# Optimization experiments

Measured on AMD Instinct MI355X. Metric: run time of the kernel, lower is better.

The kernel has to match this reference:

```python
import jax, jax.numpy as jnp
import numpy as np

# JAX reference for BERN-NN-Implicit LayerModule.forward.
# Semantics: for each output node i,
#   combined_over[i]  = sum_j relu(W)[i,j]*inputs_over[j] + (-relu(-W))[i,j]*inputs_under[j] + bias[i]
#   combined_under[i] = sum_j (-relu(-W))[i,j]*inputs_over[j] + relu(W)[i,j]*inputs_under[j] + bias[i]
# With all input Bernstein polynomials at equal degree, SumModule reduces to addition
# and prod_input_weights reduces to a weighted sum over the previous-layer neuron axis.

N_IN = 64      # previous-layer neurons
SIZE = 64      # nodes in this layer
G = 513        # Bernstein coefficient grid per dim (degree 512 + 1), dims = 2


def setup_inputs() -> dict:
    key = jax.random.key(0)
    k1, k2, k3, k4 = jax.random.split(key, 4)
    return {
        "inputs_under": jax.random.normal(k1, (N_IN, G, G), dtype=jnp.float32),
        "inputs_over": jax.random.normal(k2, (N_IN, G, G), dtype=jnp.float32),
        "weights": jax.random.normal(k3, (SIZE, N_IN), dtype=jnp.float32),
        "biases": jax.random.normal(k4, (SIZE,), dtype=jnp.float32),
        "layer_idx": 0,
    }


def reference(inputs_under, inputs_over, weights, biases, layer_idx):
    w_pos = jax.nn.relu(weights)          # [size, n_in]
    w_neg = -jax.nn.relu(-weights)        # [size, n_in]
    b = biases[:, None, None]             # [size, 1, 1]
    # [size, G, G] Bernstein coefficient grids per output node
    combined_over = (jnp.einsum("oi,ixy->oxy", w_pos, inputs_over)
                     + jnp.einsum("oi,ixy->oxy", w_neg, inputs_under)) + b
    combined_under = (jnp.einsum("oi,ixy->oxy", w_neg, inputs_over)
                      + jnp.einsum("oi,ixy->oxy", w_pos, inputs_under)) + b
    return combined_under, combined_over
```

## Files before the change

kernel.cpp:

```cpp
#include <hip/hip_runtime.h>

constexpr int PIX   = 513 * 513;
constexpr int NTILE = 128;
constexpr int NFULL = PIX / NTILE;
constexpr int GRID  = 512;

typedef short bf16x8 __attribute__((ext_vector_type(8)));
typedef float f32x4  __attribute__((ext_vector_type(4)));

__device__ __forceinline__ unsigned short f2bf(float f) {
    unsigned u = __builtin_bit_cast(unsigned, f);
    u += 0x7fffu + ((u >> 16) & 1u);
    return (unsigned short)(u >> 16);
}
__device__ __forceinline__ unsigned pack2(float a, float b) {
    return (unsigned)f2bf(a) | ((unsigned)f2bf(b) << 16);
}

__global__ __launch_bounds__(512, 2) void mfma_bounds_kernel(
    const float* __restrict__ under,
    const float* __restrict__ over,
    const float* __restrict__ W,
    const float* __restrict__ bias,
    float* __restrict__ out_under,
    float* __restrict__ out_over)
{
    __shared__ alignas(16) unsigned short Xt[2][NTILE * 128];

    const int t    = threadIdx.x;
    const int wv   = t >> 6;
    const int lane = t & 63;
    const int lrow = lane & 15;
    const int lg   = lane >> 4;
    const int m0   = wv * 16;

    bf16x8 A[4];
    {
        const int m = m0 + lrow;
        const float* wr = W + (m & 63) * 64;
        #pragma unroll
        for (int ks = 0; ks < 4; ++ks) {
            const int kbase = ks * 32 + lg * 8;
            const bool same = ((kbase < 64) == (m < 64));
            const float4 wa = *(const float4*)(wr + (kbase & 63));
            const float4 wb = *(const float4*)(wr + (kbase & 63) + 4);
            bf16x8 f;
            f[0] = (short)f2bf(same ? fmaxf(wa.x, 0.f) : fminf(wa.x, 0.f));
            f[1] = (short)f2bf(same ? fmaxf(wa.y, 0.f) : fminf(wa.y, 0.f));
            f[2] = (short)f2bf(same ? fmaxf(wa.z, 0.f) : fminf(wa.z, 0.f));
            f[3] = (short)f2bf(same ? fmaxf(wa.w, 0.f) : fminf(wa.w, 0.f));
            f[4] = (short)f2bf(same ? fmaxf(wb.x, 0.f) : fminf(wb.x, 0.f));
            f[5] = (short)f2bf(same ? fmaxf(wb.y, 0.f) : fminf(wb.y, 0.f));
            f[6] = (short)f2bf(same ? fmaxf(wb.z, 0.f) : fminf(wb.z, 0.f));
            f[7] = (short)f2bf(same ? fmaxf(wb.w, 0.f) : fminf(wb.w, 0.f));
            A[ks] = f;
        }
    }
    float bb[4];
    #pragma unroll
    for (int r = 0; r < 4; ++r)
        bb[r] = bias[(m0 + lg * 4 + r) & 63];

    const int q   = t & 31;
    const int ro  = t >> 5;
    const float* src = (ro < 8) ? over : under;
    const int rr  = (ro & 7) * 8;
    const int px0 = q * 4;
    const int kb  = ro * 16;
    const int xwr = lrow << 4;

    int tile = blockIdx.x;
    f32x4 ld[8];
    {
        const size_t pb = (size_t)tile * NTILE + px0;
        #pragma unroll
        for (int j = 0; j < 8; ++j)
            ld[j] = *(const f32x4*)(src + (size_t)(rr + j) * PIX + pb);
    }

    int cur = 0;
    while (tile < NFULL) {
        #pragma unroll
        for (int c = 0; c < 4; ++c) {
            int4 pk;
            pk.x = (int)pack2(ld[0][c], ld[1][c]);
            pk.y = (int)pack2(ld[2][c], ld[3][c]);
            pk.z = (int)pack2(ld[4][c], ld[5][c]);
            pk.w = (int)pack2(ld[6][c], ld[7][c]);
            const int px  = px0 + c;
            const int off = px * 256 + (kb ^ ((px & 15) << 4));
            *(int4*)((char*)&Xt[cur][0] + off) = pk;
        }

        const int pxbase    = tile * NTILE;
        const int tile_next = tile + GRID;

        if (tile_next < NFULL) {
            const size_t pb = (size_t)tile_next * NTILE + px0;
            #pragma unroll
            for (int j = 0; j < 8; ++j)
                ld[j] = *(const f32x4*)(src + (size_t)(rr + j) * PIX + pb);
        }

        __syncthreads();

        f32x4 acc[8];
        #pragma unroll
        for (int nt = 0; nt < 8; ++nt) {
            f32x4 v = {bb[0], bb[1], bb[2], bb[3]};
            acc[nt] = v;
        }
        #pragma unroll
        for (int nt = 0; nt < 8; ++nt) {
            const int prow = nt * 16 + lrow;
            bf16x8 Bf[4];
            #pragma unroll
            for (int ks = 0; ks < 4; ++ks) {
                const int ch = ks * 4 + lg;
                Bf[ks] = *(const bf16x8*)((const char*)&Xt[cur][0] +
                           prow * 256 + ((ch * 16) ^ xwr));
            }
            #pragma unroll
            for (int ks = 0; ks < 4; ++ks)
                acc[nt] = __builtin_amdgcn_mfma_f32_16x16x32_bf16(
                    A[ks], Bf[ks], acc[nt], 0, 0, 0);
        }

        #pragma unroll
        for (int r = 0; r < 4; ++r) {
            const int m = m0 + lg * 4 + r;
            float* base = (m < 64) ? (out_over  + (size_t)m        * PIX)
                                   : (out_under + (size_t)(m - 64) * PIX);
            #pragma unroll
            for (int nt = 0; nt < 8; ++nt)
                __builtin_nontemporal_store(acc[nt][r],
                    base + pxbase + nt * 16 + lrow);
        }

        cur ^= 1;
        tile = tile_next;
    }

    if (blockIdx.x == GRID - 1 && t < 128) {
        const int p = NFULL * NTILE;
        const int m = t;
        const int o = m & 63;
        const float* prim = (m < 64) ? over  : under;
        const float* sec  = (m < 64) ? under : over;
        float acc = bias[o];
        for (int i = 0; i < 64; ++i) {
            const float w = W[o * 64 + i];
            acc += fmaxf(w, 0.f) * prim[(size_t)i * PIX + p]
                 + fminf(w, 0.f) * sec [(size_t)i * PIX + p];
        }
        if (m < 64) out_over [(size_t)m        * PIX + p] = acc;
        else        out_under[(size_t)(m - 64) * PIX + p] = acc;
    }
}

extern "C" void kernel_launch(void* const* d_in, const int* in_sizes, int n_in,
                              void* d_out, int out_size, void* d_ws, size_t ws_size,
                              hipStream_t stream) {
    const float* under = (const float*)d_in[0];
    const float* over  = (const float*)d_in[1];
    const float* W     = (const float*)d_in[2];
    const float* bias  = (const float*)d_in[3];
    float* out_under = (float*)d_out;
    float* out_over  = out_under + (size_t)64 * PIX;

    mfma_bounds_kernel<<<GRID, 512, 0, stream>>>(under, over, W, bias,
                                                 out_under, out_over);
}
```

Before: 88.41 us.

## Warp-specialize loader and MFMA waves with fixed tiles per block

Splits each block into four producer waves that load fp32 inputs, convert them to bf16 and write them into double-buffered LDS, and four consumer waves that each compute two 16-row M tiles with MFMA and store the outputs. The grid becomes NFULL/4 blocks, each handling four consecutive tiles instead of grid-striding over 512 persistent blocks. The goal is to overlap global loads with the compute and store phases through specialization. The trade-off is that half the waves do no MFMA work, producers hold 16 registers of loads each, and there are more blocks with a short prologue each.

```diff
diff --git a/kernel.cpp b/kernel.cpp
--- a/kernel.cpp
+++ b/kernel.cpp
@@ -3,7 +3,8 @@
 constexpr int PIX   = 513 * 513;
 constexpr int NTILE = 128;
 constexpr int NFULL = PIX / NTILE;
-constexpr int GRID  = 512;
+constexpr int TPB   = 4;
+constexpr int GRID  = NFULL / TPB;
 
 typedef short bf16x8 __attribute__((ext_vector_type(8)));
 typedef float f32x4  __attribute__((ext_vector_type(4)));
@@ -27,118 +28,130 @@
 {
     __shared__ alignas(16) unsigned short Xt[2][NTILE * 128];
 
-    const int t    = threadIdx.x;
-    const int wv   = t >> 6;
-    const int lane = t & 63;
-    const int lrow = lane & 15;
-    const int lg   = lane >> 4;
-    const int m0   = wv * 16;
+    const int t   = threadIdx.x;
+    const int wv  = t >> 6;
+    const int tb0 = blockIdx.x * TPB;
 
-    bf16x8 A[4];
-    {
-        const int m = m0 + lrow;
-        const float* wr = W + (m & 63) * 64;
-        #pragma unroll
-        for (int ks = 0; ks < 4; ++ks) {
-            const int kbase = ks * 32 + lg * 8;
-            const bool same = ((kbase < 64) == (m < 64));
-            const float4 wa = *(const float4*)(wr + (kbase & 63));
-            const float4 wb = *(const float4*)(wr + (kbase & 63) + 4);
-            bf16x8 f;
-            f[0] = (short)f2bf(same ? fmaxf(wa.x, 0.f) : fminf(wa.x, 0.f));
-            f[1] = (short)f2bf(same ? fmaxf(wa.y, 0.f) : fminf(wa.y, 0.f));
-            f[2] = (short)f2bf(same ? fmaxf(wa.z, 0.f) : fminf(wa.z, 0.f));
-            f[3] = (short)f2bf(same ? fmaxf(wa.w, 0.f) : fminf(wa.w, 0.f));
-            f[4] = (short)f2bf(same ? fmaxf(wb.x, 0.f) : fminf(wb.x, 0.f));
-            f[5] = (short)f2bf(same ? fmaxf(wb.y, 0.f) : fminf(wb.y, 0.f));
-            f[6] = (short)f2bf(same ? fmaxf(wb.z, 0.f) : fminf(wb.z, 0.f));
-            f[7] = (short)f2bf(same ? fmaxf(wb.w, 0.f) : fminf(wb.w, 0.f));
-            A[ks] = f;
-        }
-    }
-    float bb[4];
-    #pragma unroll
-    for (int r = 0; r < 4; ++r)
-        bb[r] = bias[(m0 + lg * 4 + r) & 63];
+    if (wv < 4) {
+        const int q   = t & 31;
+        const int ro  = t >> 5;
+        const float* src = (ro < 4) ? over : under;
+        const int rr  = (ro & 3) * 16;
+        const int px0 = q * 4;
 
-    const int q   = t & 31;
-    const int ro  = t >> 5;
-    const float* src = (ro < 8) ? over : under;
-    const int rr  = (ro & 7) * 8;
-    const int px0 = q * 4;
-    const int kb  = ro * 16;
-    const int xwr = lrow << 4;
-
-    int tile = blockIdx.x;
-    f32x4 ld[8];
-    {
-        const size_t pb = (size_t)tile * NTILE + px0;
-        #pragma unroll
-        for (int j = 0; j < 8; ++j)
-            ld[j] = *(const f32x4*)(src + (size_t)(rr + j) * PIX + pb);
-    }
-
-    int cur = 0;
-    while (tile < NFULL) {
-        #pragma unroll
-        for (int c = 0; c < 4; ++c) {
-            int4 pk;
-            pk.x = (int)pack2(ld[0][c], ld[1][c]);
-            pk.y = (int)pack2(ld[2][c], ld[3][c]);
-            pk.z = (int)pack2(ld[4][c], ld[5][c]);
-            pk.w = (int)pack2(ld[6][c], ld[7][c]);
-            const int px  = px0 + c;
-            const int off = px * 256 + (kb ^ ((px & 15) << 4));
-            *(int4*)((char*)&Xt[cur][0] + off) = pk;
+#define STAGE(i)                                                               \
+        {                                                                      \
+            const size_t pb = (size_t)(tb0 + (i)) * NTILE + px0;               \
+            f32x4 ld[16];                                                      \
+            _Pragma("unroll")                                                  \
+            for (int j = 0; j < 16; ++j)                                       \
+                ld[j] = *(const f32x4*)(src + (size_t)(rr + j) * PIX + pb);    \
+            char* bw = (char*)&Xt[(i) & 1][0];                                 \
+            _Pragma("unroll")                                                  \
+            for (int c = 0; c < 4; ++c) {                                      \
+                const int px = px0 + c;                                        \
+                const int xw = (px & 15) << 4;                                 \
+                _Pragma("unroll")                                              \
+                for (int oct = 0; oct < 2; ++oct) {                            \
+                    int4 pk;                                                   \
+                    pk.x = (int)pack2(ld[oct*8+0][c], ld[oct*8+1][c]);         \
+                    pk.y = (int)pack2(ld[oct*8+2][c], ld[oct*8+3][c]);         \
+                    pk.z = (int)pack2(ld[oct*8+4][c], ld[oct*8+5][c]);         \
+                    pk.w = (int)pack2(ld[oct*8+6][c], ld[oct*8+7][c]);         \
+                    const int kbyte = ro * 32 + oct * 16;                      \
+                    *(int4*)(bw + px * 256 + (kbyte ^ xw)) = pk;               \
+                }                                                              \
+            }                                                                  \
         }
 
-        const int pxbase    = tile * NTILE;
-        const int tile_next = tile + GRID;
+        STAGE(0);
+        __syncthreads();
+        #pragma unroll 1
+        for (int i = 0; i < TPB; ++i) {
+            if (i + 1 < TPB) STAGE(i + 1);
+            __syncthreads();
+        }
+#undef STAGE
+    } else {
+        const int lane = t & 63;
+        const int lrow = lane & 15;
+        const int lg   = lane >> 4;
+        const int m0   = (wv - 4) * 32;
 
-        if (tile_next < NFULL) {
-            const size_t pb = (size_t)tile_next * NTILE + px0;
+        bf16x8 A[2][4];
+        #pragma unroll
+        for (int mt = 0; mt < 2; ++mt) {
+            const int m = m0 + mt * 16 + lrow;
+            const float* wr = W + (m & 63) * 64;
             #pragma unroll
-            for (int j = 0; j < 8; ++j)
-                ld[j] = *(const f32x4*)(src + (size_t)(rr + j) * PIX + pb);
+            for (int ks = 0; ks < 4; ++ks) {
+                const int kbase = ks * 32 + lg * 8;
+                const bool same = ((kbase < 64) == (m < 64));
+                const float4 wa = *(const float4*)(wr + (kbase & 63));
+                const float4 wb = *(const float4*)(wr + (kbase & 63) + 4);
+                bf16x8 f;
+                f[0] = (short)f2bf(same ? fmaxf(wa.x, 0.f) : fminf(wa.x, 0.f));
+                f[1] = (short)f2bf(same ? fmaxf(wa.y, 0.f) : fminf(wa.y, 0.f));
+                f[2] = (short)f2bf(same ? fmaxf(wa.z, 0.f) : fminf(wa.z, 0.f));
+                f[3] = (short)f2bf(same ? fmaxf(wa.w, 0.f) : fminf(wa.w, 0.f));
+                f[4] = (short)f2bf(same ? fmaxf(wb.x, 0.f) : fminf(wb.x, 0.f));
+                f[5] = (short)f2bf(same ? fmaxf(wb.y, 0.f) : fminf(wb.y, 0.f));
+                f[6] = (short)f2bf(same ? fmaxf(wb.z, 0.f) : fminf(wb.z, 0.f));
+                f[7] = (short)f2bf(same ? fmaxf(wb.w, 0.f) : fminf(wb.w, 0.f));
+                A[mt][ks] = f;
+            }
         }
+        float bb[2][4];
+        #pragma unroll
+        for (int mt = 0; mt < 2; ++mt)
+            #pragma unroll
+            for (int r = 0; r < 4; ++r)
+                bb[mt][r] = bias[(m0 + mt * 16 + lg * 4 + r) & 63];
 
         __syncthreads();
 
-        f32x4 acc[8];
-        #pragma unroll
-        for (int nt = 0; nt < 8; ++nt) {
-            f32x4 v = {bb[0], bb[1], bb[2], bb[3]};
-            acc[nt] = v;
+        const int xwr = lrow << 4;
+
+        #pragma unroll 1
+        for (int i = 0; i < TPB; ++i) {
+            const char* br   = (const char*)&Xt[i & 1][0];
+            const int pxbase = (tb0 + i) * NTILE;
+
+            #pragma unroll
+            for (int mt = 0; mt < 2; ++mt) {
+                f32x4 acc[8];
+                #pragma unroll
+                for (int nt = 0; nt < 8; ++nt) {
+                    f32x4 v = {bb[mt][0], bb[mt][1], bb[mt][2], bb[mt][3]};
+                    acc[nt] = v;
+                }
+                #pragma unroll
+                for (int nt = 0; nt < 8; ++nt) {
+                    const int prow = nt * 16 + lrow;
+                    bf16x8 Bf[4];
+                    #pragma unroll
+                    for (int ks = 0; ks < 4; ++ks) {
+                        const int ch = ks * 4 + lg;
+                        Bf[ks] = *(const bf16x8*)(br + prow * 256 + ((ch * 16) ^ xwr));
+                    }
+                    #pragma unroll
+                    for (int ks = 0; ks < 4; ++ks)
+                        acc[nt] = __builtin_amdgcn_mfma_f32_16x16x32_bf16(
+                            A[mt][ks], Bf[ks], acc[nt], 0, 0, 0);
+                }
+                #pragma unroll
+                for (int r = 0; r < 4; ++r) {
+                    const int m = m0 + mt * 16 + lg * 4 + r;
+                    float* base = (m < 64) ? (out_over  + (size_t)m        * PIX)
+                                           : (out_under + (size_t)(m - 64) * PIX);
+                    #pragma unroll
+                    for (int nt = 0; nt < 8; ++nt)
+                        __builtin_nontemporal_store(acc[nt][r],
+                            base + pxbase + nt * 16 + lrow);
+                }
+            }
+            __syncthreads();
         }
-        #pragma unroll
-        for (int nt = 0; nt < 8; ++nt) {
-            const int prow = nt * 16 + lrow;
-            bf16x8 Bf[4];
-            #pragma unroll
-            for (int ks = 0; ks < 4; ++ks) {
-                const int ch = ks * 4 + lg;
-                Bf[ks] = *(const bf16x8*)((const char*)&Xt[cur][0] +
-                           prow * 256 + ((ch * 16) ^ xwr));
-            }
-            #pragma unroll
-            for (int ks = 0; ks < 4; ++ks)
-                acc[nt] = __builtin_amdgcn_mfma_f32_16x16x32_bf16(
-                    A[ks], Bf[ks], acc[nt], 0, 0, 0);
-        }
-
-        #pragma unroll
-        for (int r = 0; r < 4; ++r) {
-            const int m = m0 + lg * 4 + r;
-            float* base = (m < 64) ? (out_over  + (size_t)m        * PIX)
-                                   : (out_under + (size_t)(m - 64) * PIX);
-            #pragma unroll
-            for (int nt = 0; nt < 8; ++nt)
-                __builtin_nontemporal_store(acc[nt][r],
-                    base + pxbase + nt * 16 + lrow);
-        }
-
-        cur ^= 1;
-        tile = tile_next;
     }
 
     if (blockIdx.x == GRID - 1 && t < 128) {
```

Result: slower. 109.5 us (+23.9%).

## Halve block size, compute two M-tiles per wave, interleave LDS packing with MFMA

Applied to the files above, without the earlier changes.

The block shrinks from 512 to 256 threads. Each wave now covers two 16-row output tiles with two sets of weight fragments, and each thread loads 16 input rows instead of 8. The main loop is restructured so that packing the next tile into the other LDS buffer is interleaved between the two MFMA compute phases. This leaves one barrier per iteration, placed after both compute and pack, aiming to overlap LDS writes and global-load latency with matrix math. In exchange, register use per thread rises (16 prefetch vectors and two accumulator sets), and each CU may hold fewer resident waves, which could reduce memory-level parallelism in this bandwidth-bound kernel.

```diff
diff --git a/kernel.cpp b/kernel.cpp
--- a/kernel.cpp
+++ b/kernel.cpp
@@ -17,7 +17,7 @@
     return (unsigned)f2bf(a) | ((unsigned)f2bf(b) << 16);
 }
 
-__global__ __launch_bounds__(512, 2) void mfma_bounds_kernel(
+__global__ __launch_bounds__(256, 2) void mfma_bounds_kernel(
     const float* __restrict__ under,
     const float* __restrict__ over,
     const float* __restrict__ W,
@@ -32,11 +32,12 @@
     const int lane = t & 63;
     const int lrow = lane & 15;
     const int lg   = lane >> 4;
-    const int m0   = wv * 16;
+    const int m0   = wv * 32;
 
-    bf16x8 A[4];
-    {
-        const int m = m0 + lrow;
+    bf16x8 A[2][4];
+    #pragma unroll
+    for (int mt = 0; mt < 2; ++mt) {
+        const int m = m0 + mt * 16 + lrow;
         const float* wr = W + (m & 63) * 64;
         #pragma unroll
         for (int ks = 0; ks < 4; ++ks) {
@@ -53,93 +54,114 @@
             f[5] = (short)f2bf(same ? fmaxf(wb.y, 0.f) : fminf(wb.y, 0.f));
             f[6] = (short)f2bf(same ? fmaxf(wb.z, 0.f) : fminf(wb.z, 0.f));
             f[7] = (short)f2bf(same ? fmaxf(wb.w, 0.f) : fminf(wb.w, 0.f));
-            A[ks] = f;
+            A[mt][ks] = f;
         }
     }
-    float bb[4];
+    float bb[2][4];
     #pragma unroll
-    for (int r = 0; r < 4; ++r)
-        bb[r] = bias[(m0 + lg * 4 + r) & 63];
+    for (int mt = 0; mt < 2; ++mt)
+        #pragma unroll
+        for (int r = 0; r < 4; ++r)
+            bb[mt][r] = bias[(m0 + mt * 16 + lg * 4 + r) & 63];
 
     const int q   = t & 31;
     const int ro  = t >> 5;
-    const float* src = (ro < 8) ? over : under;
-    const int rr  = (ro & 7) * 8;
+    const float* src = (ro < 4) ? over : under;
+    const int rr  = (ro & 3) * 16;
     const int px0 = q * 4;
-    const int kb  = ro * 16;
     const int xwr = lrow << 4;
 
+#define PACK_OCT(b, oct)                                                     \
+    {                                                                        \
+        char* bw = (char*)&Xt[(b)][0];                                       \
+        _Pragma("unroll")                                                    \
+        for (int c = 0; c < 4; ++c) {                                        \
+            const int px = px0 + c;                                          \
+            const int xw = (px & 15) << 4;                                   \
+            int4 pk;                                                         \
+            pk.x = (int)pack2(ld[(oct)*8 + 0][c], ld[(oct)*8 + 1][c]);       \
+            pk.y = (int)pack2(ld[(oct)*8 + 2][c], ld[(oct)*8 + 3][c]);       \
+            pk.z = (int)pack2(ld[(oct)*8 + 4][c], ld[(oct)*8 + 5][c]);       \
+            pk.w = (int)pack2(ld[(oct)*8 + 6][c], ld[(oct)*8 + 7][c]);       \
+            const int kbyte = ro * 32 + (oct) * 16;                          \
+            *(int4*)(bw + px * 256 + (kbyte ^ xw)) = pk;                     \
+        }                                                                    \
+    }
+
+#define COMPUTE_MT(mt)                                                       \
+    {                                                                        \
+        f32x4 acc[8];                                                        \
+        _Pragma("unroll")                                                    \
+        for (int nt = 0; nt < 8; ++nt) {                                     \
+            f32x4 v = {bb[mt][0], bb[mt][1], bb[mt][2], bb[mt][3]};          \
+            acc[nt] = v;                                                     \
+        }                                                                    \
+        _Pragma("unroll")                                                    \
+        for (int nt = 0; nt < 8; ++nt) {                                     \
+            const int prow = nt * 16 + lrow;                                 \
+            bf16x8 Bf[4];                                                    \
+            _Pragma("unroll")                                                \
+            for (int ks = 0; ks < 4; ++ks) {                                 \
+                const int ch = ks * 4 + lg;                                  \
+                Bf[ks] = *(const bf16x8*)(br + prow * 256 + ((ch * 16) ^ xwr)); \
+            }                                                                \
+            _Pragma("unroll")                                                \
+            for (int ks = 0; ks < 4; ++ks)                                   \
+                acc[nt] = __builtin_amdgcn_mfma_f32_16x16x32_bf16(           \
+                    A[mt][ks], Bf[ks], acc[nt], 0, 0, 0);                    \
+        }                                                                    \
+        _Pragma("unroll")                                                    \
+        for (int r = 0; r < 4; ++r) {                                        \
+            const int m = m0 + (mt) * 16 + lg * 4 + r;                       \
+            float* base = (m < 64) ? (out_over  + (size_t)m        * PIX)    \
+                                   : (out_under + (size_t)(m - 64) * PIX);   \
+            _Pragma("unroll")                                                \
+            for (int nt = 0; nt < 8; ++nt)                                   \
+                __builtin_nontemporal_store(acc[nt][r],                      \
+                    base + pxbase + nt * 16 + lrow);                         \
+        }                                                                    \
+    }
+
     int tile = blockIdx.x;
-    f32x4 ld[8];
     {
+        f32x4 ld[16];
         const size_t pb = (size_t)tile * NTILE + px0;
         #pragma unroll
-        for (int j = 0; j < 8; ++j)
+        for (int j = 0; j < 16; ++j)
             ld[j] = *(const f32x4*)(src + (size_t)(rr + j) * PIX + pb);
+        PACK_OCT(0, 0);
+        PACK_OCT(0, 1);
     }
+    __syncthreads();
 
     int cur = 0;
-    while (tile < NFULL) {
-        #pragma unroll
-        for (int c = 0; c < 4; ++c) {
-            int4 pk;
-            pk.x = (int)pack2(ld[0][c], ld[1][c]);
-            pk.y = (int)pack2(ld[2][c], ld[3][c]);
-            pk.z = (int)pack2(ld[4][c], ld[5][c]);
-            pk.w = (int)pack2(ld[6][c], ld[7][c]);
-            const int px  = px0 + c;
-            const int off = px * 256 + (kb ^ ((px & 15) << 4));
-            *(int4*)((char*)&Xt[cur][0] + off) = pk;
-        }
+    for (;;) {
+        const int tnext = tile + GRID;
+        const bool more = tnext < NFULL;
 
-        const int pxbase    = tile * NTILE;
-        const int tile_next = tile + GRID;
-
-        if (tile_next < NFULL) {
-            const size_t pb = (size_t)tile_next * NTILE + px0;
+        f32x4 ld[16];
+        if (more) {
+            const size_t pb = (size_t)tnext * NTILE + px0;
             #pragma unroll
-            for (int j = 0; j < 8; ++j)
+            for (int j = 0; j < 16; ++j)
                 ld[j] = *(const f32x4*)(src + (size_t)(rr + j) * PIX + pb);
         }
 
+        const int pxbase = tile * NTILE;
+        const char* br = (const char*)&Xt[cur][0];
+
+        COMPUTE_MT(0);
+        if (more) PACK_OCT(cur ^ 1, 0);
+        COMPUTE_MT(1);
+        if (more) PACK_OCT(cur ^ 1, 1);
+
         __syncthreads();
-
-        f32x4 acc[8];
-        #pragma unroll
-        for (int nt = 0; nt < 8; ++nt) {
-            f32x4 v = {bb[0], bb[1], bb[2], bb[3]};
-            acc[nt] = v;
-        }
-        #pragma unroll
-        for (int nt = 0; nt < 8; ++nt) {
-            const int prow = nt * 16 + lrow;
-            bf16x8 Bf[4];
-            #pragma unroll
-            for (int ks = 0; ks < 4; ++ks) {
-                const int ch = ks * 4 + lg;
-                Bf[ks] = *(const bf16x8*)((const char*)&Xt[cur][0] +
-                           prow * 256 + ((ch * 16) ^ xwr));
-            }
-            #pragma unroll
-            for (int ks = 0; ks < 4; ++ks)
-                acc[nt] = __builtin_amdgcn_mfma_f32_16x16x32_bf16(
-                    A[ks], Bf[ks], acc[nt], 0, 0, 0);
-        }
-
-        #pragma unroll
-        for (int r = 0; r < 4; ++r) {
-            const int m = m0 + lg * 4 + r;
-            float* base = (m < 64) ? (out_over  + (size_t)m        * PIX)
-                                   : (out_under + (size_t)(m - 64) * PIX);
-            #pragma unroll
-            for (int nt = 0; nt < 8; ++nt)
-                __builtin_nontemporal_store(acc[nt][r],
-                    base + pxbase + nt * 16 + lrow);
-        }
-
+        if (!more) break;
         cur ^= 1;
-        tile = tile_next;
+        tile = tnext;
     }
+#undef PACK_OCT
+#undef COMPUTE_MT
 
     if (blockIdx.x == GRID - 1 && t < 128) {
         const int p = NFULL * NTILE;
@@ -168,6 +190,6 @@
     float* out_under = (float*)d_out;
     float* out_over  = out_under + (size_t)64 * PIX;
 
-    mfma_bounds_kernel<<<GRID, 512, 0, stream>>>(under, over, W, bias,
+    mfma_bounds_kernel<<<GRID, 256, 0, stream>>>(under, over, W, bias,
                                                  out_under, out_over);
 }
```

After: 95.52 us. 1.08x slower.
